# Performance work log

Hardware: AMD Instinct MI355X
Metric: run time of the kernel (lower is better)

## Reference

```python
import jax, jax.numpy as jnp
import numpy as np

EPS = 1e-8

def prelu(x, a):
    return jnp.where(x >= 0, x, a * x)

def setup_inputs() -> dict:
    key = jax.random.key(0)
    ks = jax.random.split(key, 8)
    B, G, N, T = 4, 8, 128, 6000
    H = 384
    x = jax.random.normal(ks[0], (B, G, N, T), dtype=jnp.float32)
    # torch.nn.Linear default init: U(-1/sqrt(fan_in), 1/sqrt(fan_in))
    def lin(k, out_f, in_f):
        k1, k2 = jax.random.split(k)
        bound = 1.0 / np.sqrt(in_f)
        W = jax.random.uniform(k1, (out_f, in_f), minval=-bound, maxval=bound, dtype=jnp.float32)
        b = jax.random.uniform(k2, (out_f,), minval=-bound, maxval=bound, dtype=jnp.float32)
        return W, b
    Wi, bi = lin(ks[1], H, N)
    Wm, bm = lin(ks[2], H, H)
    Wo, bo = lin(ks[3], N, 2 * H)
    # PReLU default: single learnable scalar initialized to 0.25
    ai = jnp.float32(0.25)
    am = jnp.float32(0.25)
    ao = jnp.float32(0.25)
    gamma = jnp.ones((N,), dtype=jnp.float32)
    beta = jnp.zeros((N,), dtype=jnp.float32)
    return {"input": x, "Wi": Wi, "bi": bi, "ai": ai, "Wm": Wm, "bm": bm, "am": am,
            "Wo": Wo, "bo": bo, "ao": ao, "gamma": gamma, "beta": beta}

def reference(input, Wi, bi, ai, Wm, bm, am, Wo, bo, ao, gamma, beta):
    B, G, N, T = input.shape
    # [B, T, G, N]
    h = jnp.transpose(input, (0, 3, 1, 2))
    # TAC_input: Linear(N->H) + PReLU
    gi = prelu(jnp.einsum('btgn,hn->btgh', h, Wi) + bi, ai)          # [B,T,G,H]
    # mean over groups, TAC_mean: Linear(H->H) + PReLU
    gm = gi.mean(axis=2)                                              # [B,T,H]
    gm = prelu(jnp.einsum('bth,oh->bto', gm, Wm) + bm, am)            # [B,T,H]
    gm = jnp.broadcast_to(gm[:, :, None, :], gi.shape)                # [B,T,G,H]
    cat = jnp.concatenate([gi, gm], axis=-1)                          # [B,T,G,2H]
    # TAC_output: Linear(2H->N) + PReLU
    go = prelu(jnp.einsum('btgc,nc->btgn', cat, Wo) + bo, ao)         # [B,T,G,N]
    go = jnp.transpose(go, (0, 2, 3, 1))                              # [B,G,N,T]
    # GlobLN over (N, T) per (batch*G) sample, affine along channel N
    mean = go.mean(axis=(2, 3), keepdims=True)
    var = jnp.mean((go - mean) ** 2, axis=(2, 3), keepdims=True)
    normed = (go - mean) / jnp.sqrt(var + EPS)
    go = gamma[None, None, :, None] * normed + beta[None, None, :, None]
    return input + go
```

## Files before the change

kernel.cpp:

```cpp
#include <hip/hip_runtime.h>

typedef __bf16 bf16_t;
typedef __bf16 bf16x8 __attribute__((ext_vector_type(8)));
typedef float f32x4 __attribute__((ext_vector_type(4)));

static constexpr int Bq = 4, Gg = 8, Nn = 128, Tt = 6000, Hh = 384;
static constexpr int TB = 16;
static constexpr int MR = TB * Gg;
static constexpr int LDA = 136;
static constexpr int LDG = 392;
static constexpr int LDSM = 392;
static constexpr int LDV = 132;

static constexpr size_t OFF_WI  = 0;
static constexpr size_t OFF_WM  = OFF_WI + (size_t)Hh * Nn * 2;
static constexpr size_t OFF_WO  = OFF_WM + (size_t)Hh * Hh * 2;
static constexpr size_t OFF_ST  = OFF_WO + (size_t)Nn * 2 * Hh * 2;
static constexpr size_t OFF_MRS = OFF_ST + 64 * 2 * 4;
static constexpr size_t OFF_GO  = (size_t)1 << 20;
static constexpr size_t WS_NEED = OFF_GO + (size_t)Bq * Tt * Gg * Nn * 2;

static constexpr int SM_SM = 0;
static constexpr int SM_MM = 12544;
static constexpr int SM_VV = 25088;
static constexpr int SM_GI = 34816;
static constexpr int SM_STT = 135168;
static constexpr int SMEM_BYTES = 135232;

#define MFMA16(a, b, c) __builtin_amdgcn_mfma_f32_16x16x32_bf16((a), (b), (c), 0, 0, 0)

__global__ void k0_prep(const float* __restrict__ Wi, const float* __restrict__ Wm,
                        const float* __restrict__ Wo,
                        bf16_t* __restrict__ WiB, bf16_t* __restrict__ WmB,
                        bf16_t* __restrict__ WoB, float* __restrict__ stats) {
    int i = blockIdx.x * blockDim.x + threadIdx.x;
    const int n1 = Hh * Nn, n2 = Hh * Hh, n3 = Nn * 2 * Hh;
    for (int idx = i; idx < n1 + n2 + n3; idx += gridDim.x * blockDim.x) {
        if (idx < n1)            WiB[idx] = (bf16_t)Wi[idx];
        else if (idx < n1 + n2)  WmB[idx - n1] = (bf16_t)Wm[idx - n1];
        else                     WoB[idx - n1 - n2] = (bf16_t)Wo[idx - n1 - n2];
    }
    if (i < 128) stats[i] = 0.f;
}

__device__ __forceinline__ int as_col(int row, int c) {
    return ((((c >> 3) ^ ((row >> 3) & 7)) << 3) | (c & 7));
}

__global__ __launch_bounds__(512, 2)
void k1_fused(const float* __restrict__ x,
              const bf16_t* __restrict__ WiB, const float* __restrict__ bi, const float* __restrict__ aip,
              const bf16_t* __restrict__ WmB, const float* __restrict__ bm, const float* __restrict__ amp,
              const bf16_t* __restrict__ WoB, const float* __restrict__ bo, const float* __restrict__ aop,
              bf16_t* __restrict__ go, float* __restrict__ stats) {
    extern __shared__ char smem[];
    bf16_t* As = (bf16_t*)(smem);
    bf16_t* Sm = (bf16_t*)(smem + SM_SM);
    bf16_t* Mm = (bf16_t*)(smem + SM_MM);
    float*  Vv = (float*)(smem + SM_VV);
    bf16_t* Gi = (bf16_t*)(smem + SM_GI);
    float*  st = (float*)(smem + SM_STT);

    const int tid  = threadIdx.x;
    const int lane = tid & 63;
    const int w    = tid >> 6;
    const int l15  = lane & 15;
    const int l4   = lane >> 4;
    const int mh   = w >> 2;
    const int ws4  = w & 3;
    const int b    = blockIdx.x / (Tt / TB);
    const int t0   = (blockIdx.x % (Tt / TB)) * TB;

    if (tid < 16) st[tid] = 0.f;

    for (int idx = tid; idx < MR * Nn; idx += 512) {
        int tl = idx & 15;
        int gn = idx >> 4;
        int g = gn >> 7;
        int n = gn & 127;
        float v = x[((size_t)((b * Gg + g) * Nn + n)) * Tt + t0 + tl];
        int row = tl * Gg + g;
        As[row * LDA + as_col(row, n)] = (bf16_t)v;
    }
    __syncthreads();

    const float ai = aip[0], am = amp[0], ao = aop[0];

    {
        const int cb = ws4 * 96;
        f32x4 acc[4][6];
        #pragma unroll
        for (int mt = 0; mt < 4; mt++)
            #pragma unroll
            for (int ni = 0; ni < 6; ni++) acc[mt][ni] = f32x4{0.f, 0.f, 0.f, 0.f};
        #pragma unroll
        for (int kk = 0; kk < 4; kk++) {
            const int k0 = kk * 32 + l4 * 8;
            bf16x8 a[4], bb[6];
            #pragma unroll
            for (int ni = 0; ni < 6; ni++)
                bb[ni] = *(const bf16x8*)&WiB[(cb + ni * 16 + l15) * Nn + k0];
            #pragma unroll
            for (int mt = 0; mt < 4; mt++) {
                int row = mh * 64 + mt * 16 + l15;
                a[mt] = *(const bf16x8*)&As[row * LDA + as_col(row, k0)];
            }
            #pragma unroll
            for (int mt = 0; mt < 4; mt++)
                #pragma unroll
                for (int ni = 0; ni < 6; ni++)
                    acc[mt][ni] = MFMA16(a[mt], bb[ni], acc[mt][ni]);
        }
        #pragma unroll
        for (int ni = 0; ni < 6; ni++) {
            int col = cb + ni * 16 + l15;
            float bv = bi[col];
            #pragma unroll
            for (int mt = 0; mt < 4; mt++) {
                #pragma unroll
                for (int j = 0; j < 4; j++) {
                    int row = mh * 64 + mt * 16 + l4 * 4 + j;
                    float v = acc[mt][ni][j] + bv;
                    v = v >= 0.f ? v : ai * v;
                    Gi[row * LDG + col] = (bf16_t)v;
                }
            }
        }
    }
    __syncthreads();

    for (int idx = tid; idx < TB * (Hh / 8); idx += 512) {
        int tl = idx / (Hh / 8);
        int h0 = (idx - tl * (Hh / 8)) * 8;
        float s[8];
        #pragma unroll
        for (int e = 0; e < 8; e++) s[e] = 0.f;
        #pragma unroll
        for (int g = 0; g < 8; g++) {
            bf16x8 vv = *(const bf16x8*)&Gi[(tl * 8 + g) * LDG + h0];
            #pragma unroll
            for (int e = 0; e < 8; e++) s[e] += (float)vv[e];
        }
        bf16x8 o;
        #pragma unroll
        for (int e = 0; e < 8; e++) o[e] = (bf16_t)(0.125f * s[e]);
        *(bf16x8*)&Sm[tl * LDSM + h0] = o;
    }
    __syncthreads();

    {
        const int cb2 = w * 48;
        f32x4 acc2[3];
        #pragma unroll
        for (int ni = 0; ni < 3; ni++) acc2[ni] = f32x4{0.f, 0.f, 0.f, 0.f};
        #pragma unroll
        for (int kk = 0; kk < 12; kk++) {
            const int k0 = kk * 32 + l4 * 8;
            bf16x8 a = *(const bf16x8*)&Sm[l15 * LDSM + k0];
            #pragma unroll
            for (int ni = 0; ni < 3; ni++) {
                bf16x8 bb = *(const bf16x8*)&WmB[(cb2 + ni * 16 + l15) * Hh + k0];
                acc2[ni] = MFMA16(a, bb, acc2[ni]);
            }
        }
        #pragma unroll
        for (int ni = 0; ni < 3; ni++) {
            int col = cb2 + ni * 16 + l15;
            float bv = bm[col];
            #pragma unroll
            for (int j = 0; j < 4; j++) {
                float v = acc2[ni][j] + bv;
                v = v >= 0.f ? v : am * v;
                Mm[(l4 * 4 + j) * LDSM + col] = (bf16_t)v;
            }
        }
    }
    __syncthreads();

    {
        const int nblk = w * 16;
        f32x4 acc3 = f32x4{0.f, 0.f, 0.f, 0.f};
        #pragma unroll
        for (int kk = 0; kk < 12; kk++) {
            const int k0 = kk * 32 + l4 * 8;
            bf16x8 a = *(const bf16x8*)&Mm[l15 * LDSM + k0];
            bf16x8 bb = *(const bf16x8*)&WoB[(nblk + l15) * 768 + 384 + k0];
            acc3 = MFMA16(a, bb, acc3);
        }
        #pragma unroll
        for (int j = 0; j < 4; j++) Vv[(l4 * 4 + j) * LDV + nblk + l15] = acc3[j];
    }
    __syncthreads();

    {
        const int cb4 = ws4 * 32;
        f32x4 acc4[4][2];
        #pragma unroll
        for (int mt = 0; mt < 4; mt++)
            #pragma unroll
            for (int ni = 0; ni < 2; ni++) acc4[mt][ni] = f32x4{0.f, 0.f, 0.f, 0.f};
        #pragma unroll
        for (int kk = 0; kk < 12; kk++) {
            const int k0 = kk * 32 + l4 * 8;
            bf16x8 b0 = *(const bf16x8*)&WoB[(cb4 + l15) * 768 + k0];
            bf16x8 b1 = *(const bf16x8*)&WoB[(cb4 + 16 + l15) * 768 + k0];
            bf16x8 a[4];
            #pragma unroll
            for (int mt = 0; mt < 4; mt++)
                a[mt] = *(const bf16x8*)&Gi[(mh * 64 + mt * 16 + l15) * LDG + k0];
            #pragma unroll
            for (int mt = 0; mt < 4; mt++) {
                acc4[mt][0] = MFMA16(a[mt], b0, acc4[mt][0]);
                acc4[mt][1] = MFMA16(a[mt], b1, acc4[mt][1]);
            }
        }
        float gsum[4] = {0.f, 0.f, 0.f, 0.f};
        float gss[4]  = {0.f, 0.f, 0.f, 0.f};
        #pragma unroll
        for (int ni = 0; ni < 2; ni++) {
            int col = cb4 + ni * 16 + l15;
            float bv = bo[col];
            #pragma unroll
            for (int mt = 0; mt < 4; mt++) {
                #pragma unroll
                for (int j = 0; j < 4; j++) {
                    int row = mh * 64 + mt * 16 + l4 * 4 + j;
                    int tl = row >> 3;
                    int g = row & 7;
                    float v = acc4[mt][ni][j] + Vv[tl * LDV + col] + bv;
                    v = v >= 0.f ? v : ao * v;
                    go[((size_t)((b * Tt + t0 + tl) * Gg + g)) * Nn + col] = (bf16_t)v;
                    gsum[j] += v;
                    gss[j] += v * v;
                }
            }
        }
        #pragma unroll
        for (int j = 0; j < 4; j++) {
            float s = gsum[j], q = gss[j];
            #pragma unroll
            for (int off = 1; off < 16; off <<= 1) {
                s += __shfl_xor(s, off, 64);
                q += __shfl_xor(q, off, 64);
            }
            if (l15 == 0) {
                int g = (l4 * 4 + j) & 7;
                atomicAdd(&st[g * 2 + 0], s);
                atomicAdd(&st[g * 2 + 1], q);
            }
        }
    }
    __syncthreads();
    if (tid < 16) atomicAdd(&stats[b * 16 + tid], st[tid]);
}

__global__ void k_final(const float* __restrict__ stats, float* __restrict__ mr) {
    int i = threadIdx.x;
    if (i < 64) {
        const float cnt = (float)Nn * (float)Tt;
        float mean = stats[i * 2] / cnt;
        float var = stats[i * 2 + 1] / cnt - mean * mean;
        mr[i * 2] = mean;
        mr[i * 2 + 1] = rsqrtf(var + 1e-8f);
    }
}

__global__ __launch_bounds__(256)
void k_apply(const float* __restrict__ x, const bf16_t* __restrict__ go,
             const float* __restrict__ mr, const float* __restrict__ gamma,
             const float* __restrict__ beta, float* __restrict__ out) {
    __shared__ float tr[32][65];
    int bid = blockIdx.x;
    const int tt = bid % 94; bid /= 94;
    const int nn = bid & 3;  bid >>= 2;
    const int g = bid & 7;
    const int b = bid >> 3;
    const int t0 = tt * 64, n0 = nn * 32;
    const int tid = threadIdx.x;
    const float mean = mr[(b * 8 + g) * 2], rstd = mr[(b * 8 + g) * 2 + 1];

    for (int idx = tid; idx < 2048; idx += 256) {
        int nl = idx & 31, tl = idx >> 5;
        int t = t0 + tl;
        float v = 0.f;
        if (t < Tt) v = (float)go[((size_t)((b * Tt + t) * Gg + g)) * Nn + n0 + nl];
        tr[nl][tl] = v;
    }
    __syncthreads();
    for (int idx = tid; idx < 2048; idx += 256) {
        int tl = idx & 63, nl = idx >> 6;
        int t = t0 + tl;
        if (t < Tt) {
            int n = n0 + nl;
            size_t a = ((size_t)((b * Gg + g) * Nn + n)) * Tt + t;
            out[a] = x[a] + gamma[n] * (tr[nl][tl] - mean) * rstd + beta[n];
        }
    }
}

extern "C" void kernel_launch(void* const* d_in, const int* in_sizes, int n_in,
                              void* d_out, int out_size, void* d_ws, size_t ws_size,
                              hipStream_t stream) {
    const float* x     = (const float*)d_in[0];
    const float* Wi    = (const float*)d_in[1];
    const float* bi    = (const float*)d_in[2];
    const float* ai    = (const float*)d_in[3];
    const float* Wm    = (const float*)d_in[4];
    const float* bm    = (const float*)d_in[5];
    const float* am    = (const float*)d_in[6];
    const float* Wo    = (const float*)d_in[7];
    const float* bo    = (const float*)d_in[8];
    const float* ao    = (const float*)d_in[9];
    const float* gamma = (const float*)d_in[10];
    const float* beta  = (const float*)d_in[11];
    float* out = (float*)d_out;
    char* ws = (char*)d_ws;

    if (ws_size < WS_NEED) return;

    bf16_t* WiB  = (bf16_t*)(ws + OFF_WI);
    bf16_t* WmB  = (bf16_t*)(ws + OFF_WM);
    bf16_t* WoB  = (bf16_t*)(ws + OFF_WO);
    float*  stat = (float*)(ws + OFF_ST);
    float*  mrs  = (float*)(ws + OFF_MRS);
    bf16_t* goB  = (bf16_t*)(ws + OFF_GO);

    k0_prep<<<dim3(512), dim3(256), 0, stream>>>(Wi, Wm, Wo, WiB, WmB, WoB, stat);
    k1_fused<<<dim3(Bq * (Tt / TB)), dim3(512), SMEM_BYTES, stream>>>(
        x, WiB, bi, ai, WmB, bm, am, WoB, bo, ao, goB, stat);
    k_final<<<dim3(1), dim3(64), 0, stream>>>(stat, mrs);
    k_apply<<<dim3(Bq * Gg * 4 * 94), dim3(256), 0, stream>>>(x, goB, mrs, gamma, beta, out);
}
```

Measured before the change: 254.8 us.

## Halve time tile per block and replace global atomics with per-block partial sums

Reduces the per-block time tile from 16 to 8 steps, which halves shared memory use and raises the occupancy target to 4 blocks per CU. It also doubles the block count, improving load balance. Small MFMA tiles in the mean and output stages now waste half their rows, and the weight matrices are re-read by twice as many blocks. Global atomic accumulation of the norm statistics is replaced by per-block partial writes, reduced in a single 1024-thread final kernel, which also removes the stats zeroing from the prep kernel.

```diff
diff --git a/kernel.cpp b/kernel.cpp
--- a/kernel.cpp
+++ b/kernel.cpp
@@ -5,8 +5,9 @@
 typedef float f32x4 __attribute__((ext_vector_type(4)));
 
 static constexpr int Bq = 4, Gg = 8, Nn = 128, Tt = 6000, Hh = 384;
-static constexpr int TB = 16;
+static constexpr int TB = 8;
 static constexpr int MR = TB * Gg;
+static constexpr int NBLK = Tt / TB;
 static constexpr int LDA = 136;
 static constexpr int LDG = 392;
 static constexpr int LDSM = 392;
@@ -15,24 +16,24 @@
 static constexpr size_t OFF_WI  = 0;
 static constexpr size_t OFF_WM  = OFF_WI + (size_t)Hh * Nn * 2;
 static constexpr size_t OFF_WO  = OFF_WM + (size_t)Hh * Hh * 2;
-static constexpr size_t OFF_ST  = OFF_WO + (size_t)Nn * 2 * Hh * 2;
-static constexpr size_t OFF_MRS = OFF_ST + 64 * 2 * 4;
+static constexpr size_t OFF_PT  = OFF_WO + (size_t)Nn * 2 * Hh * 2;
+static constexpr size_t OFF_MRS = OFF_PT + (size_t)Bq * NBLK * 16 * 4;
 static constexpr size_t OFF_GO  = (size_t)1 << 20;
 static constexpr size_t WS_NEED = OFF_GO + (size_t)Bq * Tt * Gg * Nn * 2;
 
-static constexpr int SM_SM = 0;
-static constexpr int SM_MM = 12544;
-static constexpr int SM_VV = 25088;
-static constexpr int SM_GI = 34816;
-static constexpr int SM_STT = 135168;
-static constexpr int SMEM_BYTES = 135232;
+static constexpr int SM_SM  = 0;
+static constexpr int SM_MM  = 6272;
+static constexpr int SM_VV  = 12544;
+static constexpr int SM_GI  = 17408;
+static constexpr int SM_STT = 67584;
+static constexpr int SMEM_BYTES = 67648;
 
 #define MFMA16(a, b, c) __builtin_amdgcn_mfma_f32_16x16x32_bf16((a), (b), (c), 0, 0, 0)
 
 __global__ void k0_prep(const float* __restrict__ Wi, const float* __restrict__ Wm,
                         const float* __restrict__ Wo,
                         bf16_t* __restrict__ WiB, bf16_t* __restrict__ WmB,
-                        bf16_t* __restrict__ WoB, float* __restrict__ stats) {
+                        bf16_t* __restrict__ WoB) {
     int i = blockIdx.x * blockDim.x + threadIdx.x;
     const int n1 = Hh * Nn, n2 = Hh * Hh, n3 = Nn * 2 * Hh;
     for (int idx = i; idx < n1 + n2 + n3; idx += gridDim.x * blockDim.x) {
@@ -40,19 +41,18 @@
         else if (idx < n1 + n2)  WmB[idx - n1] = (bf16_t)Wm[idx - n1];
         else                     WoB[idx - n1 - n2] = (bf16_t)Wo[idx - n1 - n2];
     }
-    if (i < 128) stats[i] = 0.f;
 }
 
 __device__ __forceinline__ int as_col(int row, int c) {
     return ((((c >> 3) ^ ((row >> 3) & 7)) << 3) | (c & 7));
 }
 
-__global__ __launch_bounds__(512, 2)
+__global__ __launch_bounds__(512, 4)
 void k1_fused(const float* __restrict__ x,
               const bf16_t* __restrict__ WiB, const float* __restrict__ bi, const float* __restrict__ aip,
               const bf16_t* __restrict__ WmB, const float* __restrict__ bm, const float* __restrict__ amp,
               const bf16_t* __restrict__ WoB, const float* __restrict__ bo, const float* __restrict__ aop,
-              bf16_t* __restrict__ go, float* __restrict__ stats) {
+              bf16_t* __restrict__ go, float* __restrict__ part) {
     extern __shared__ char smem[];
     bf16_t* As = (bf16_t*)(smem);
     bf16_t* Sm = (bf16_t*)(smem + SM_SM);
@@ -68,14 +68,14 @@
     const int l4   = lane >> 4;
     const int mh   = w >> 2;
     const int ws4  = w & 3;
-    const int b    = blockIdx.x / (Tt / TB);
-    const int t0   = (blockIdx.x % (Tt / TB)) * TB;
+    const int b    = blockIdx.x / NBLK;
+    const int t0   = (blockIdx.x % NBLK) * TB;
 
     if (tid < 16) st[tid] = 0.f;
 
     for (int idx = tid; idx < MR * Nn; idx += 512) {
-        int tl = idx & 15;
-        int gn = idx >> 4;
+        int tl = idx & 7;
+        int gn = idx >> 3;
         int g = gn >> 7;
         int n = gn & 127;
         float v = x[((size_t)((b * Gg + g) * Nn + n)) * Tt + t0 + tl];
@@ -88,25 +88,25 @@
 
     {
         const int cb = ws4 * 96;
-        f32x4 acc[4][6];
-        #pragma unroll
-        for (int mt = 0; mt < 4; mt++)
+        f32x4 acc[2][6];
+        #pragma unroll
+        for (int mt = 0; mt < 2; mt++)
             #pragma unroll
             for (int ni = 0; ni < 6; ni++) acc[mt][ni] = f32x4{0.f, 0.f, 0.f, 0.f};
         #pragma unroll
         for (int kk = 0; kk < 4; kk++) {
             const int k0 = kk * 32 + l4 * 8;
-            bf16x8 a[4], bb[6];
+            bf16x8 a[2], bb[6];
             #pragma unroll
             for (int ni = 0; ni < 6; ni++)
                 bb[ni] = *(const bf16x8*)&WiB[(cb + ni * 16 + l15) * Nn + k0];
             #pragma unroll
-            for (int mt = 0; mt < 4; mt++) {
-                int row = mh * 64 + mt * 16 + l15;
+            for (int mt = 0; mt < 2; mt++) {
+                int row = mh * 32 + mt * 16 + l15;
                 a[mt] = *(const bf16x8*)&As[row * LDA + as_col(row, k0)];
             }
             #pragma unroll
-            for (int mt = 0; mt < 4; mt++)
+            for (int mt = 0; mt < 2; mt++)
                 #pragma unroll
                 for (int ni = 0; ni < 6; ni++)
                     acc[mt][ni] = MFMA16(a[mt], bb[ni], acc[mt][ni]);
@@ -116,10 +116,10 @@
             int col = cb + ni * 16 + l15;
             float bv = bi[col];
             #pragma unroll
-            for (int mt = 0; mt < 4; mt++) {
+            for (int mt = 0; mt < 2; mt++) {
                 #pragma unroll
                 for (int j = 0; j < 4; j++) {
-                    int row = mh * 64 + mt * 16 + l4 * 4 + j;
+                    int row = mh * 32 + mt * 16 + l4 * 4 + j;
                     float v = acc[mt][ni][j] + bv;
                     v = v >= 0.f ? v : ai * v;
                     Gi[row * LDG + col] = (bf16_t)v;
@@ -156,22 +156,24 @@
         #pragma unroll
         for (int kk = 0; kk < 12; kk++) {
             const int k0 = kk * 32 + l4 * 8;
-            bf16x8 a = *(const bf16x8*)&Sm[l15 * LDSM + k0];
+            bf16x8 a = *(const bf16x8*)&Sm[(l15 & 7) * LDSM + k0];
             #pragma unroll
             for (int ni = 0; ni < 3; ni++) {
                 bf16x8 bb = *(const bf16x8*)&WmB[(cb2 + ni * 16 + l15) * Hh + k0];
                 acc2[ni] = MFMA16(a, bb, acc2[ni]);
             }
         }
-        #pragma unroll
-        for (int ni = 0; ni < 3; ni++) {
-            int col = cb2 + ni * 16 + l15;
-            float bv = bm[col];
-            #pragma unroll
-            for (int j = 0; j < 4; j++) {
-                float v = acc2[ni][j] + bv;
-                v = v >= 0.f ? v : am * v;
-                Mm[(l4 * 4 + j) * LDSM + col] = (bf16_t)v;
+        if (l4 < 2) {
+            #pragma unroll
+            for (int ni = 0; ni < 3; ni++) {
+                int col = cb2 + ni * 16 + l15;
+                float bv = bm[col];
+                #pragma unroll
+                for (int j = 0; j < 4; j++) {
+                    float v = acc2[ni][j] + bv;
+                    v = v >= 0.f ? v : am * v;
+                    Mm[(l4 * 4 + j) * LDSM + col] = (bf16_t)v;
+                }
             }
         }
     }
@@ -183,20 +185,22 @@
         #pragma unroll
         for (int kk = 0; kk < 12; kk++) {
             const int k0 = kk * 32 + l4 * 8;
-            bf16x8 a = *(const bf16x8*)&Mm[l15 * LDSM + k0];
+            bf16x8 a = *(const bf16x8*)&Mm[(l15 & 7) * LDSM + k0];
             bf16x8 bb = *(const bf16x8*)&WoB[(nblk + l15) * 768 + 384 + k0];
             acc3 = MFMA16(a, bb, acc3);
         }
-        #pragma unroll
-        for (int j = 0; j < 4; j++) Vv[(l4 * 4 + j) * LDV + nblk + l15] = acc3[j];
+        if (l4 < 2) {
+            #pragma unroll
+            for (int j = 0; j < 4; j++) Vv[(l4 * 4 + j) * LDV + nblk + l15] = acc3[j];
+        }
     }
     __syncthreads();
 
     {
         const int cb4 = ws4 * 32;
-        f32x4 acc4[4][2];
-        #pragma unroll
-        for (int mt = 0; mt < 4; mt++)
+        f32x4 acc4[2][2];
+        #pragma unroll
+        for (int mt = 0; mt < 2; mt++)
             #pragma unroll
             for (int ni = 0; ni < 2; ni++) acc4[mt][ni] = f32x4{0.f, 0.f, 0.f, 0.f};
         #pragma unroll
@@ -204,12 +208,12 @@
             const int k0 = kk * 32 + l4 * 8;
             bf16x8 b0 = *(const bf16x8*)&WoB[(cb4 + l15) * 768 + k0];
             bf16x8 b1 = *(const bf16x8*)&WoB[(cb4 + 16 + l15) * 768 + k0];
-            bf16x8 a[4];
-            #pragma unroll
-            for (int mt = 0; mt < 4; mt++)
-                a[mt] = *(const bf16x8*)&Gi[(mh * 64 + mt * 16 + l15) * LDG + k0];
-            #pragma unroll
-            for (int mt = 0; mt < 4; mt++) {
+            bf16x8 a[2];
+            #pragma unroll
+            for (int mt = 0; mt < 2; mt++)
+                a[mt] = *(const bf16x8*)&Gi[(mh * 32 + mt * 16 + l15) * LDG + k0];
+            #pragma unroll
+            for (int mt = 0; mt < 2; mt++) {
                 acc4[mt][0] = MFMA16(a[mt], b0, acc4[mt][0]);
                 acc4[mt][1] = MFMA16(a[mt], b1, acc4[mt][1]);
             }
@@ -221,10 +225,10 @@
             int col = cb4 + ni * 16 + l15;
             float bv = bo[col];
             #pragma unroll
-            for (int mt = 0; mt < 4; mt++) {
+            for (int mt = 0; mt < 2; mt++) {
                 #pragma unroll
                 for (int j = 0; j < 4; j++) {
-                    int row = mh * 64 + mt * 16 + l4 * 4 + j;
+                    int row = mh * 32 + mt * 16 + l4 * 4 + j;
                     int tl = row >> 3;
                     int g = row & 7;
                     float v = acc4[mt][ni][j] + Vv[tl * LDV + col] + bv;
@@ -251,17 +255,39 @@
         }
     }
     __syncthreads();
-    if (tid < 16) atomicAdd(&stats[b * 16 + tid], st[tid]);
-}
-
-__global__ void k_final(const float* __restrict__ stats, float* __restrict__ mr) {
-    int i = threadIdx.x;
-    if (i < 64) {
-        const float cnt = (float)Nn * (float)Tt;
-        float mean = stats[i * 2] / cnt;
-        float var = stats[i * 2 + 1] / cnt - mean * mean;
-        mr[i * 2] = mean;
-        mr[i * 2 + 1] = rsqrtf(var + 1e-8f);
+    if (tid < 16) part[(size_t)blockIdx.x * 16 + tid] = st[tid];
+}
+
+__global__ __launch_bounds__(1024)
+void k_final(const float* __restrict__ part, float* __restrict__ mr) {
+    __shared__ float red[64][17];
+    const int tid = threadIdx.x;
+    const int key = tid & 63;
+    const int chunk = tid >> 6;
+    const int bb = key >> 4;
+    const int t0 = chunk * 47;
+    const int cnt = min(47, NBLK - t0);
+    float s = 0.f;
+    for (int i = 0; i < cnt; i++)
+        s += part[(size_t)(bb * NBLK + t0 + i) * 16 + (key & 15)];
+    red[key][chunk] = s;
+    __syncthreads();
+    if (tid < 64) {
+        float tot = 0.f;
+        #pragma unroll
+        for (int ch = 0; ch < 16; ch++) tot += red[tid][ch];
+        red[tid][16] = tot;
+    }
+    __syncthreads();
+    if (tid < 32) {
+        int b2 = tid >> 3, g2 = tid & 7;
+        float s0 = red[b2 * 16 + g2 * 2][16];
+        float s1 = red[b2 * 16 + g2 * 2 + 1][16];
+        const float cntf = (float)Nn * (float)Tt;
+        float mean = s0 / cntf;
+        float var = s1 / cntf - mean * mean;
+        mr[tid * 2] = mean;
+        mr[tid * 2 + 1] = rsqrtf(var + 1e-8f);
     }
 }
 
@@ -321,13 +347,13 @@
     bf16_t* WiB  = (bf16_t*)(ws + OFF_WI);
     bf16_t* WmB  = (bf16_t*)(ws + OFF_WM);
     bf16_t* WoB  = (bf16_t*)(ws + OFF_WO);
-    float*  stat = (float*)(ws + OFF_ST);
+    float*  prt  = (float*)(ws + OFF_PT);
     float*  mrs  = (float*)(ws + OFF_MRS);
     bf16_t* goB  = (bf16_t*)(ws + OFF_GO);
 
-    k0_prep<<<dim3(512), dim3(256), 0, stream>>>(Wi, Wm, Wo, WiB, WmB, WoB, stat);
-    k1_fused<<<dim3(Bq * (Tt / TB)), dim3(512), SMEM_BYTES, stream>>>(
-        x, WiB, bi, ai, WmB, bm, am, WoB, bo, ao, goB, stat);
-    k_final<<<dim3(1), dim3(64), 0, stream>>>(stat, mrs);
+    k0_prep<<<dim3(512), dim3(256), 0, stream>>>(Wi, Wm, Wo, WiB, WmB, WoB);
+    k1_fused<<<dim3(Bq * NBLK), dim3(512), SMEM_BYTES, stream>>>(
+        x, WiB, bi, ai, WmB, bm, am, WoB, bo, ao, goB, prt);
+    k_final<<<dim3(1), dim3(1024), 0, stream>>>(prt, mrs);
     k_apply<<<dim3(Bq * Gg * 4 * 94), dim3(256), 0, stream>>>(x, goB, mrs, gamma, beta, out);
 }
```

Measured after the change: 367.4 us. +44.1%, slower.

## Split fused TAC kernel into three GEMM stages with global intermediates

Applied to the files above, without the earlier changes.

Replaces the single large-shared-memory fused kernel with three kernels: first-layer GEMM plus group mean, a mid kernel for the mean-branch GEMMs, and the output GEMM that writes per-tile partial statistics instead of atomics. Intermediates gi, gm and v now go through global workspace, processed in chunks sized to the available workspace, with the old fused path kept as a fallback. The aim is to free LDS and raise occupancy and MFMA utilisation per stage, at the cost of extra global traffic for the gi intermediate and more launches.

```diff
diff --git a/kernel.cpp b/kernel.cpp
--- a/kernel.cpp
+++ b/kernel.cpp
@@ -6,26 +6,23 @@
 
 static constexpr int Bq = 4, Gg = 8, Nn = 128, Tt = 6000, Hh = 384;
 static constexpr int TB = 16;
-static constexpr int MR = TB * Gg;
+static constexpr int NTPB = Tt / TB;
+static constexpr int NTILES = Bq * NTPB;
 static constexpr int LDA = 136;
-static constexpr int LDG = 392;
-static constexpr int LDSM = 392;
-static constexpr int LDV = 132;
+static constexpr int LDMM = 392;
 
 static constexpr size_t OFF_WI  = 0;
 static constexpr size_t OFF_WM  = OFF_WI + (size_t)Hh * Nn * 2;
 static constexpr size_t OFF_WO  = OFF_WM + (size_t)Hh * Hh * 2;
-static constexpr size_t OFF_ST  = OFF_WO + (size_t)Nn * 2 * Hh * 2;
-static constexpr size_t OFF_MRS = OFF_ST + 64 * 2 * 4;
-static constexpr size_t OFF_GO  = (size_t)1 << 20;
-static constexpr size_t WS_NEED = OFF_GO + (size_t)Bq * Tt * Gg * Nn * 2;
-
-static constexpr int SM_SM = 0;
-static constexpr int SM_MM = 12544;
-static constexpr int SM_VV = 25088;
-static constexpr int SM_GI = 34816;
-static constexpr int SM_STT = 135168;
-static constexpr int SMEM_BYTES = 135232;
+static constexpr size_t OFF_PT  = OFF_WO + (size_t)Nn * 2 * Hh * 2;
+static constexpr size_t OFF_MRS = OFF_PT + (size_t)NTILES * 4 * 16 * 4;
+static constexpr size_t OFF_GM  = (size_t)1 << 20;
+static constexpr size_t OFF_V   = OFF_GM + (size_t)Bq * Tt * Hh * 2;
+static constexpr size_t OFF_GO  = OFF_V + (size_t)Bq * Tt * Nn * 4;
+static constexpr size_t OFF_GI  = OFF_GO + (size_t)Bq * Tt * Gg * Nn * 2;
+static constexpr size_t GI_BYTES_FULL = (size_t)NTILES * 128 * Hh * 2;
+static constexpr size_t OFF_GO_FB = (size_t)1 << 20;
+static constexpr size_t WS_FB = OFF_GO_FB + (size_t)Bq * Tt * Gg * Nn * 2;
 
 #define MFMA16(a, b, c) __builtin_amdgcn_mfma_f32_16x16x32_bf16((a), (b), (c), 0, 0, 0)
 
@@ -47,221 +44,237 @@
     return ((((c >> 3) ^ ((row >> 3) & 7)) << 3) | (c & 7));
 }
 
-__global__ __launch_bounds__(512, 2)
-void k1_fused(const float* __restrict__ x,
-              const bf16_t* __restrict__ WiB, const float* __restrict__ bi, const float* __restrict__ aip,
-              const bf16_t* __restrict__ WmB, const float* __restrict__ bm, const float* __restrict__ amp,
-              const bf16_t* __restrict__ WoB, const float* __restrict__ bo, const float* __restrict__ aop,
-              bf16_t* __restrict__ go, float* __restrict__ stats) {
-    extern __shared__ char smem[];
-    bf16_t* As = (bf16_t*)(smem);
-    bf16_t* Sm = (bf16_t*)(smem + SM_SM);
-    bf16_t* Mm = (bf16_t*)(smem + SM_MM);
-    float*  Vv = (float*)(smem + SM_VV);
-    bf16_t* Gi = (bf16_t*)(smem + SM_GI);
-    float*  st = (float*)(smem + SM_STT);
-
-    const int tid  = threadIdx.x;
-    const int lane = tid & 63;
-    const int w    = tid >> 6;
-    const int l15  = lane & 15;
-    const int l4   = lane >> 4;
-    const int mh   = w >> 2;
-    const int ws4  = w & 3;
-    const int b    = blockIdx.x / (Tt / TB);
-    const int t0   = (blockIdx.x % (Tt / TB)) * TB;
-
-    if (tid < 16) st[tid] = 0.f;
-
-    for (int idx = tid; idx < MR * Nn; idx += 512) {
-        int tl = idx & 15;
-        int gn = idx >> 4;
-        int g = gn >> 7;
-        int n = gn & 127;
-        float v = x[((size_t)((b * Gg + g) * Nn + n)) * Tt + t0 + tl];
-        int row = tl * Gg + g;
-        As[row * LDA + as_col(row, n)] = (bf16_t)v;
-    }
-    __syncthreads();
-
-    const float ai = aip[0], am = amp[0], ao = aop[0];
+__global__ __launch_bounds__(512, 4)
+void kA_gemm1(const float* __restrict__ x, const bf16_t* __restrict__ WiB,
+              const float* __restrict__ bi, const float* __restrict__ aip,
+              bf16_t* __restrict__ gi, bf16_t* __restrict__ gm, int tile0) {
+    __shared__ bf16_t As[128 * LDA];
+    const int tid = threadIdx.x, lane = tid & 63, w = tid >> 6;
+    const int l15 = lane & 15, l4 = lane >> 4;
+    const int tile = tile0 + blockIdx.x;
+    const int b = tile / NTPB, t0 = (tile % NTPB) * TB;
 
     {
-        const int cb = ws4 * 96;
-        f32x4 acc[4][6];
-        #pragma unroll
-        for (int mt = 0; mt < 4; mt++)
-            #pragma unroll
-            for (int ni = 0; ni < 6; ni++) acc[mt][ni] = f32x4{0.f, 0.f, 0.f, 0.f};
-        #pragma unroll
-        for (int kk = 0; kk < 4; kk++) {
-            const int k0 = kk * 32 + l4 * 8;
-            bf16x8 a[4], bb[6];
-            #pragma unroll
-            for (int ni = 0; ni < 6; ni++)
-                bb[ni] = *(const bf16x8*)&WiB[(cb + ni * 16 + l15) * Nn + k0];
-            #pragma unroll
-            for (int mt = 0; mt < 4; mt++) {
-                int row = mh * 64 + mt * 16 + l15;
-                a[mt] = *(const bf16x8*)&As[row * LDA + as_col(row, k0)];
-            }
-            #pragma unroll
-            for (int mt = 0; mt < 4; mt++)
+        const int g0 = tid >> 7, n0 = tid & 127;
+        #pragma unroll
+        for (int h = 0; h < 2; h++) {
+            int gg = g0 + 4 * h;
+            #pragma unroll
+            for (int q = 0; q < 4; q++) {
+                f32x4 xv = *(const f32x4*)&x[((size_t)((b * Gg + gg) * Nn + n0)) * Tt + t0 + 4 * q];
                 #pragma unroll
-                for (int ni = 0; ni < 6; ni++)
-                    acc[mt][ni] = MFMA16(a[mt], bb[ni], acc[mt][ni]);
-        }
-        #pragma unroll
-        for (int ni = 0; ni < 6; ni++) {
-            int col = cb + ni * 16 + l15;
-            float bv = bi[col];
-            #pragma unroll
-            for (int mt = 0; mt < 4; mt++) {
-                #pragma unroll
-                for (int j = 0; j < 4; j++) {
-                    int row = mh * 64 + mt * 16 + l4 * 4 + j;
-                    float v = acc[mt][ni][j] + bv;
-                    v = v >= 0.f ? v : ai * v;
-                    Gi[row * LDG + col] = (bf16_t)v;
+                for (int e = 0; e < 4; e++) {
+                    int row = (q * 4 + e) * Gg + gg;
+                    As[row * LDA + as_col(row, n0)] = (bf16_t)xv[e];
                 }
             }
         }
     }
     __syncthreads();
 
-    for (int idx = tid; idx < TB * (Hh / 8); idx += 512) {
-        int tl = idx / (Hh / 8);
-        int h0 = (idx - tl * (Hh / 8)) * 8;
-        float s[8];
-        #pragma unroll
-        for (int e = 0; e < 8; e++) s[e] = 0.f;
-        #pragma unroll
-        for (int g = 0; g < 8; g++) {
-            bf16x8 vv = *(const bf16x8*)&Gi[(tl * 8 + g) * LDG + h0];
-            #pragma unroll
-            for (int e = 0; e < 8; e++) s[e] += (float)vv[e];
-        }
-        bf16x8 o;
-        #pragma unroll
-        for (int e = 0; e < 8; e++) o[e] = (bf16_t)(0.125f * s[e]);
-        *(bf16x8*)&Sm[tl * LDSM + h0] = o;
-    }
-    __syncthreads();
-
-    {
-        const int cb2 = w * 48;
-        f32x4 acc2[3];
-        #pragma unroll
-        for (int ni = 0; ni < 3; ni++) acc2[ni] = f32x4{0.f, 0.f, 0.f, 0.f};
-        #pragma unroll
-        for (int kk = 0; kk < 12; kk++) {
-            const int k0 = kk * 32 + l4 * 8;
-            bf16x8 a = *(const bf16x8*)&Sm[l15 * LDSM + k0];
-            #pragma unroll
-            for (int ni = 0; ni < 3; ni++) {
-                bf16x8 bb = *(const bf16x8*)&WmB[(cb2 + ni * 16 + l15) * Hh + k0];
-                acc2[ni] = MFMA16(a, bb, acc2[ni]);
-            }
-        }
-        #pragma unroll
-        for (int ni = 0; ni < 3; ni++) {
-            int col = cb2 + ni * 16 + l15;
-            float bv = bm[col];
+    const float ai = aip[0];
+    const int cb = w * 48;
+    f32x4 acc[8][3];
+    #pragma unroll
+    for (int mt = 0; mt < 8; mt++)
+        #pragma unroll
+        for (int nc = 0; nc < 3; nc++) acc[mt][nc] = f32x4{0.f, 0.f, 0.f, 0.f};
+    #pragma unroll
+    for (int kk = 0; kk < 4; kk++) {
+        const int k0 = kk * 32 + l4 * 8;
+        bf16x8 bb[3];
+        #pragma unroll
+        for (int nc = 0; nc < 3; nc++)
+            bb[nc] = *(const bf16x8*)&WiB[(cb + nc * 16 + l15) * Nn + k0];
+        #pragma unroll
+        for (int mt = 0; mt < 8; mt++) {
+            int row = mt * 16 + l15;
+            bf16x8 a = *(const bf16x8*)&As[row * LDA + as_col(row, k0)];
+            #pragma unroll
+            for (int nc = 0; nc < 3; nc++) acc[mt][nc] = MFMA16(a, bb[nc], acc[mt][nc]);
+        }
+    }
+    const size_t giBase = (size_t)blockIdx.x * 128 * Hh;
+    #pragma unroll
+    for (int nc = 0; nc < 3; nc++) {
+        int col = cb + nc * 16 + l15;
+        float bv = bi[col];
+        #pragma unroll
+        for (int mt = 0; mt < 8; mt++) {
+            float ms = 0.f;
             #pragma unroll
             for (int j = 0; j < 4; j++) {
-                float v = acc2[ni][j] + bv;
-                v = v >= 0.f ? v : am * v;
-                Mm[(l4 * 4 + j) * LDSM + col] = (bf16_t)v;
-            }
-        }
-    }
-    __syncthreads();
-
-    {
-        const int nblk = w * 16;
-        f32x4 acc3 = f32x4{0.f, 0.f, 0.f, 0.f};
-        #pragma unroll
-        for (int kk = 0; kk < 12; kk++) {
-            const int k0 = kk * 32 + l4 * 8;
-            bf16x8 a = *(const bf16x8*)&Mm[l15 * LDSM + k0];
-            bf16x8 bb = *(const bf16x8*)&WoB[(nblk + l15) * 768 + 384 + k0];
-            acc3 = MFMA16(a, bb, acc3);
-        }
-        #pragma unroll
-        for (int j = 0; j < 4; j++) Vv[(l4 * 4 + j) * LDV + nblk + l15] = acc3[j];
-    }
-    __syncthreads();
-
-    {
-        const int cb4 = ws4 * 32;
-        f32x4 acc4[4][2];
-        #pragma unroll
-        for (int mt = 0; mt < 4; mt++)
-            #pragma unroll
-            for (int ni = 0; ni < 2; ni++) acc4[mt][ni] = f32x4{0.f, 0.f, 0.f, 0.f};
-        #pragma unroll
-        for (int kk = 0; kk < 12; kk++) {
-            const int k0 = kk * 32 + l4 * 8;
-            bf16x8 b0 = *(const bf16x8*)&WoB[(cb4 + l15) * 768 + k0];
-            bf16x8 b1 = *(const bf16x8*)&WoB[(cb4 + 16 + l15) * 768 + k0];
-            bf16x8 a[4];
-            #pragma unroll
-            for (int mt = 0; mt < 4; mt++)
-                a[mt] = *(const bf16x8*)&Gi[(mh * 64 + mt * 16 + l15) * LDG + k0];
-            #pragma unroll
-            for (int mt = 0; mt < 4; mt++) {
-                acc4[mt][0] = MFMA16(a[mt], b0, acc4[mt][0]);
-                acc4[mt][1] = MFMA16(a[mt], b1, acc4[mt][1]);
-            }
-        }
-        float gsum[4] = {0.f, 0.f, 0.f, 0.f};
-        float gss[4]  = {0.f, 0.f, 0.f, 0.f};
-        #pragma unroll
-        for (int ni = 0; ni < 2; ni++) {
-            int col = cb4 + ni * 16 + l15;
-            float bv = bo[col];
-            #pragma unroll
-            for (int mt = 0; mt < 4; mt++) {
-                #pragma unroll
-                for (int j = 0; j < 4; j++) {
-                    int row = mh * 64 + mt * 16 + l4 * 4 + j;
-                    int tl = row >> 3;
-                    int g = row & 7;
-                    float v = acc4[mt][ni][j] + Vv[tl * LDV + col] + bv;
-                    v = v >= 0.f ? v : ao * v;
-                    go[((size_t)((b * Tt + t0 + tl) * Gg + g)) * Nn + col] = (bf16_t)v;
-                    gsum[j] += v;
-                    gss[j] += v * v;
-                }
-            }
-        }
+                int row = mt * 16 + l4 * 4 + j;
+                float v = acc[mt][nc][j] + bv;
+                v = v >= 0.f ? v : ai * v;
+                gi[giBase + (size_t)row * Hh + col] = (bf16_t)v;
+                ms += v;
+            }
+            ms += __shfl_xor(ms, 16, 64);
+            if ((l4 & 1) == 0) {
+                int tl = mt * 2 + (l4 >> 1);
+                gm[((size_t)tile * TB + tl) * Hh + col] = (bf16_t)(0.125f * ms);
+            }
+        }
+    }
+}
+
+__global__ __launch_bounds__(256, 2)
+void kB_mid(const bf16_t* __restrict__ gm, const bf16_t* __restrict__ WmB,
+            const float* __restrict__ bm, const float* __restrict__ amp,
+            const bf16_t* __restrict__ WoB, float* __restrict__ v,
+            int tile0, int ntilesC) {
+    __shared__ bf16_t MmS[4][16 * LDMM];
+    const int tid = threadIdx.x, lane = tid & 63, w = tid >> 6;
+    const int l15 = lane & 15, l4 = lane >> 4;
+    const int tileL = blockIdx.x * 4 + w;
+    if (tileL >= ntilesC) return;
+    const int row0 = (tile0 + tileL) * TB;
+    bf16_t* Mm = MmS[w];
+
+    f32x4 acc2[24];
+    #pragma unroll
+    for (int nc = 0; nc < 24; nc++) acc2[nc] = f32x4{0.f, 0.f, 0.f, 0.f};
+    #pragma unroll
+    for (int ks = 0; ks < 12; ks++) {
+        const int k0 = ks * 32 + l4 * 8;
+        bf16x8 a = *(const bf16x8*)&gm[((size_t)row0 + l15) * Hh + k0];
+        #pragma unroll
+        for (int nc = 0; nc < 24; nc++) {
+            bf16x8 bb = *(const bf16x8*)&WmB[(nc * 16 + l15) * Hh + k0];
+            acc2[nc] = MFMA16(a, bb, acc2[nc]);
+        }
+    }
+    const float am = amp[0];
+    #pragma unroll
+    for (int nc = 0; nc < 24; nc++) {
+        int col = nc * 16 + l15;
+        float bv = bm[col];
         #pragma unroll
         for (int j = 0; j < 4; j++) {
-            float s = gsum[j], q = gss[j];
-            #pragma unroll
-            for (int off = 1; off < 16; off <<= 1) {
-                s += __shfl_xor(s, off, 64);
-                q += __shfl_xor(q, off, 64);
-            }
-            if (l15 == 0) {
-                int g = (l4 * 4 + j) & 7;
-                atomicAdd(&st[g * 2 + 0], s);
-                atomicAdd(&st[g * 2 + 1], q);
-            }
-        }
-    }
-    __syncthreads();
-    if (tid < 16) atomicAdd(&stats[b * 16 + tid], st[tid]);
-}
-
-__global__ void k_final(const float* __restrict__ stats, float* __restrict__ mr) {
-    int i = threadIdx.x;
-    if (i < 64) {
-        const float cnt = (float)Nn * (float)Tt;
-        float mean = stats[i * 2] / cnt;
-        float var = stats[i * 2 + 1] / cnt - mean * mean;
-        mr[i * 2] = mean;
-        mr[i * 2 + 1] = rsqrtf(var + 1e-8f);
+            float vv = acc2[nc][j] + bv;
+            vv = vv >= 0.f ? vv : am * vv;
+            Mm[(l4 * 4 + j) * LDMM + col] = (bf16_t)vv;
+        }
+    }
+    f32x4 acc3[8];
+    #pragma unroll
+    for (int nc = 0; nc < 8; nc++) acc3[nc] = f32x4{0.f, 0.f, 0.f, 0.f};
+    #pragma unroll
+    for (int ks = 0; ks < 12; ks++) {
+        const int k0 = ks * 32 + l4 * 8;
+        bf16x8 a = *(const bf16x8*)&Mm[l15 * LDMM + k0];
+        #pragma unroll
+        for (int nc = 0; nc < 8; nc++) {
+            bf16x8 bb = *(const bf16x8*)&WoB[(nc * 16 + l15) * 768 + 384 + k0];
+            acc3[nc] = MFMA16(a, bb, acc3[nc]);
+        }
+    }
+    #pragma unroll
+    for (int nc = 0; nc < 8; nc++) {
+        int col = nc * 16 + l15;
+        #pragma unroll
+        for (int j = 0; j < 4; j++)
+            v[((size_t)row0 + l4 * 4 + j) * Nn + col] = acc3[nc][j];
+    }
+}
+
+__global__ __launch_bounds__(256, 3)
+void kC_gemm4(const bf16_t* __restrict__ gi, const float* __restrict__ v,
+              const bf16_t* __restrict__ WoB, const float* __restrict__ bo,
+              const float* __restrict__ aop, bf16_t* __restrict__ go,
+              float* __restrict__ part, int tile0) {
+    const int tid = threadIdx.x, lane = tid & 63, w = tid >> 6;
+    const int l15 = lane & 15, l4 = lane >> 4;
+    const int tile = tile0 + blockIdx.x;
+    const size_t rL0 = (size_t)blockIdx.x * 128 + w * 32;
+    const size_t Rg0 = (size_t)tile * 128 + w * 32;
+
+    f32x4 acc[2][8];
+    #pragma unroll
+    for (int mt = 0; mt < 2; mt++)
+        #pragma unroll
+        for (int nc = 0; nc < 8; nc++) acc[mt][nc] = f32x4{0.f, 0.f, 0.f, 0.f};
+    #pragma unroll
+    for (int ks = 0; ks < 12; ks++) {
+        const int k0 = ks * 32 + l4 * 8;
+        bf16x8 bb[8];
+        #pragma unroll
+        for (int nc = 0; nc < 8; nc++)
+            bb[nc] = *(const bf16x8*)&WoB[(nc * 16 + l15) * 768 + k0];
+        #pragma unroll
+        for (int mt = 0; mt < 2; mt++) {
+            bf16x8 a = *(const bf16x8*)&gi[(rL0 + mt * 16 + l15) * Hh + k0];
+            #pragma unroll
+            for (int nc = 0; nc < 8; nc++) acc[mt][nc] = MFMA16(a, bb[nc], acc[mt][nc]);
+        }
+    }
+    const float ao = aop[0];
+    float gsum[4] = {0.f, 0.f, 0.f, 0.f};
+    float gss[4]  = {0.f, 0.f, 0.f, 0.f};
+    #pragma unroll
+    for (int nc = 0; nc < 8; nc++) {
+        int col = nc * 16 + l15;
+        float bv = bo[col];
+        #pragma unroll
+        for (int mt = 0; mt < 2; mt++) {
+            #pragma unroll
+            for (int j = 0; j < 4; j++) {
+                size_t Rg = Rg0 + mt * 16 + l4 * 4 + j;
+                float val = acc[mt][nc][j] + v[(Rg >> 3) * Nn + col] + bv;
+                val = val >= 0.f ? val : ao * val;
+                go[Rg * Nn + col] = (bf16_t)val;
+                gsum[j] += val;
+                gss[j] += val * val;
+            }
+        }
+    }
+    #pragma unroll
+    for (int j = 0; j < 4; j++) {
+        float s = gsum[j], q = gss[j];
+        #pragma unroll
+        for (int off = 1; off < 16; off <<= 1) {
+            s += __shfl_xor(s, off, 64);
+            q += __shfl_xor(q, off, 64);
+        }
+        s += __shfl_xor(s, 32, 64);
+        q += __shfl_xor(q, 32, 64);
+        if (l15 == 0 && l4 < 2) {
+            int g = l4 * 4 + j;
+            part[((size_t)tile * 4 + w) * 16 + g * 2 + 0] = s;
+            part[((size_t)tile * 4 + w) * 16 + g * 2 + 1] = q;
+        }
+    }
+}
+
+__global__ __launch_bounds__(1024)
+void k_final_split(const float* __restrict__ part, float* __restrict__ mr) {
+    __shared__ float red[64][17];
+    const int tid = threadIdx.x, key = tid & 63, chunk = tid >> 6;
+    const int bb = key >> 4;
+    const int t0 = chunk * 94;
+    const int cnt = min(94, 1500 - t0);
+    float s = 0.f;
+    for (int i = 0; i < cnt; i++)
+        s += part[(size_t)(bb * 1500 + t0 + i) * 16 + (key & 15)];
+    red[key][chunk] = s;
+    __syncthreads();
+    if (tid < 64) {
+        float tot = 0.f;
+        #pragma unroll
+        for (int ch = 0; ch < 16; ch++) tot += red[tid][ch];
+        red[tid][16] = tot;
+    }
+    __syncthreads();
+    if (tid < 32) {
+        int b2 = tid >> 3, g2 = tid & 7;
+        float s0 = red[b2 * 16 + g2 * 2][16];
+        float s1 = red[b2 * 16 + g2 * 2 + 1][16];
+        const float cntf = (float)Nn * (float)Tt;
+        float mean = s0 / cntf;
+        float var = s1 / cntf - mean * mean;
+        mr[tid * 2] = mean;
+        mr[tid * 2 + 1] = rsqrtf(var + 1e-8f);
     }
 }
 
@@ -295,6 +308,206 @@
             size_t a = ((size_t)((b * Gg + g) * Nn + n)) * Tt + t;
             out[a] = x[a] + gamma[n] * (tr[nl][tl] - mean) * rstd + beta[n];
         }
+    }
+}
+
+static constexpr int FB_LDA = 136, FB_LDG = 392, FB_LDSM = 392, FB_LDV = 132;
+static constexpr int FB_SM_SM = 0, FB_SM_MM = 12544, FB_SM_VV = 25088,
+                     FB_SM_GI = 34816, FB_SM_STT = 135168, FB_SMEM = 135232;
+
+__global__ __launch_bounds__(512, 2)
+void k1_fused_fb(const float* __restrict__ x,
+                 const bf16_t* __restrict__ WiB, const float* __restrict__ bi, const float* __restrict__ aip,
+                 const bf16_t* __restrict__ WmB, const float* __restrict__ bm, const float* __restrict__ amp,
+                 const bf16_t* __restrict__ WoB, const float* __restrict__ bo, const float* __restrict__ aop,
+                 bf16_t* __restrict__ go, float* __restrict__ stats) {
+    extern __shared__ char smem[];
+    bf16_t* As = (bf16_t*)(smem);
+    bf16_t* Sm = (bf16_t*)(smem + FB_SM_SM);
+    bf16_t* Mm = (bf16_t*)(smem + FB_SM_MM);
+    float*  Vv = (float*)(smem + FB_SM_VV);
+    bf16_t* Gi = (bf16_t*)(smem + FB_SM_GI);
+    float*  st = (float*)(smem + FB_SM_STT);
+    const int tid = threadIdx.x, lane = tid & 63, w = tid >> 6;
+    const int l15 = lane & 15, l4 = lane >> 4, mh = w >> 2, ws4 = w & 3;
+    const int b = blockIdx.x / NTPB, t0 = (blockIdx.x % NTPB) * TB;
+    if (tid < 16) st[tid] = 0.f;
+    for (int idx = tid; idx < 128 * Nn; idx += 512) {
+        int tl = idx & 15, gn = idx >> 4, g = gn >> 7, n = gn & 127;
+        float v = x[((size_t)((b * Gg + g) * Nn + n)) * Tt + t0 + tl];
+        int row = tl * Gg + g;
+        As[row * FB_LDA + as_col(row, n)] = (bf16_t)v;
+    }
+    __syncthreads();
+    const float ai = aip[0], am = amp[0], ao = aop[0];
+    {
+        const int cb = ws4 * 96;
+        f32x4 acc[4][6];
+        #pragma unroll
+        for (int mt = 0; mt < 4; mt++)
+            #pragma unroll
+            for (int ni = 0; ni < 6; ni++) acc[mt][ni] = f32x4{0.f, 0.f, 0.f, 0.f};
+        #pragma unroll
+        for (int kk = 0; kk < 4; kk++) {
+            const int k0 = kk * 32 + l4 * 8;
+            bf16x8 a[4], bb[6];
+            #pragma unroll
+            for (int ni = 0; ni < 6; ni++)
+                bb[ni] = *(const bf16x8*)&WiB[(cb + ni * 16 + l15) * Nn + k0];
+            #pragma unroll
+            for (int mt = 0; mt < 4; mt++) {
+                int row = mh * 64 + mt * 16 + l15;
+                a[mt] = *(const bf16x8*)&As[row * FB_LDA + as_col(row, k0)];
+            }
+            #pragma unroll
+            for (int mt = 0; mt < 4; mt++)
+                #pragma unroll
+                for (int ni = 0; ni < 6; ni++)
+                    acc[mt][ni] = MFMA16(a[mt], bb[ni], acc[mt][ni]);
+        }
+        #pragma unroll
+        for (int ni = 0; ni < 6; ni++) {
+            int col = cb + ni * 16 + l15;
+            float bv = bi[col];
+            #pragma unroll
+            for (int mt = 0; mt < 4; mt++)
+                #pragma unroll
+                for (int j = 0; j < 4; j++) {
+                    int row = mh * 64 + mt * 16 + l4 * 4 + j;
+                    float v = acc[mt][ni][j] + bv;
+                    v = v >= 0.f ? v : ai * v;
+                    Gi[row * FB_LDG + col] = (bf16_t)v;
+                }
+        }
+    }
+    __syncthreads();
+    for (int idx = tid; idx < TB * (Hh / 8); idx += 512) {
+        int tl = idx / (Hh / 8), h0 = (idx - tl * (Hh / 8)) * 8;
+        float s[8];
+        #pragma unroll
+        for (int e = 0; e < 8; e++) s[e] = 0.f;
+        #pragma unroll
+        for (int g = 0; g < 8; g++) {
+            bf16x8 vv = *(const bf16x8*)&Gi[(tl * 8 + g) * FB_LDG + h0];
+            #pragma unroll
+            for (int e = 0; e < 8; e++) s[e] += (float)vv[e];
+        }
+        bf16x8 o;
+        #pragma unroll
+        for (int e = 0; e < 8; e++) o[e] = (bf16_t)(0.125f * s[e]);
+        *(bf16x8*)&Sm[tl * FB_LDSM + h0] = o;
+    }
+    __syncthreads();
+    {
+        const int cb2 = w * 48;
+        f32x4 acc2[3];
+        #pragma unroll
+        for (int ni = 0; ni < 3; ni++) acc2[ni] = f32x4{0.f, 0.f, 0.f, 0.f};
+        #pragma unroll
+        for (int kk = 0; kk < 12; kk++) {
+            const int k0 = kk * 32 + l4 * 8;
+            bf16x8 a = *(const bf16x8*)&Sm[l15 * FB_LDSM + k0];
+            #pragma unroll
+            for (int ni = 0; ni < 3; ni++) {
+                bf16x8 bb = *(const bf16x8*)&WmB[(cb2 + ni * 16 + l15) * Hh + k0];
+                acc2[ni] = MFMA16(a, bb, acc2[ni]);
+            }
+        }
+        #pragma unroll
+        for (int ni = 0; ni < 3; ni++) {
+            int col = cb2 + ni * 16 + l15;
+            float bv = bm[col];
+            #pragma unroll
+            for (int j = 0; j < 4; j++) {
+                float v = acc2[ni][j] + bv;
+                v = v >= 0.f ? v : am * v;
+                Mm[(l4 * 4 + j) * FB_LDSM + col] = (bf16_t)v;
+            }
+        }
+    }
+    __syncthreads();
+    {
+        const int nblk = w * 16;
+        f32x4 acc3 = f32x4{0.f, 0.f, 0.f, 0.f};
+        #pragma unroll
+        for (int kk = 0; kk < 12; kk++) {
+            const int k0 = kk * 32 + l4 * 8;
+            bf16x8 a = *(const bf16x8*)&Mm[l15 * FB_LDSM + k0];
+            bf16x8 bb = *(const bf16x8*)&WoB[(nblk + l15) * 768 + 384 + k0];
+            acc3 = MFMA16(a, bb, acc3);
+        }
+        #pragma unroll
+        for (int j = 0; j < 4; j++) Vv[(l4 * 4 + j) * FB_LDV + nblk + l15] = acc3[j];
+    }
+    __syncthreads();
+    {
+        const int cb4 = ws4 * 32;
+        f32x4 acc4[4][2];
+        #pragma unroll
+        for (int mt = 0; mt < 4; mt++)
+            #pragma unroll
+            for (int ni = 0; ni < 2; ni++) acc4[mt][ni] = f32x4{0.f, 0.f, 0.f, 0.f};
+        #pragma unroll
+        for (int kk = 0; kk < 12; kk++) {
+            const int k0 = kk * 32 + l4 * 8;
+            bf16x8 b0 = *(const bf16x8*)&WoB[(cb4 + l15) * 768 + k0];
+            bf16x8 b1 = *(const bf16x8*)&WoB[(cb4 + 16 + l15) * 768 + k0];
+            bf16x8 a[4];
+            #pragma unroll
+            for (int mt = 0; mt < 4; mt++)
+                a[mt] = *(const bf16x8*)&Gi[(mh * 64 + mt * 16 + l15) * FB_LDG + k0];
+            #pragma unroll
+            for (int mt = 0; mt < 4; mt++) {
+                acc4[mt][0] = MFMA16(a[mt], b0, acc4[mt][0]);
+                acc4[mt][1] = MFMA16(a[mt], b1, acc4[mt][1]);
+            }
+        }
+        float gsum[4] = {0.f, 0.f, 0.f, 0.f};
+        float gss[4]  = {0.f, 0.f, 0.f, 0.f};
+        #pragma unroll
+        for (int ni = 0; ni < 2; ni++) {
+            int col = cb4 + ni * 16 + l15;
+            float bv = bo[col];
+            #pragma unroll
+            for (int mt = 0; mt < 4; mt++)
+                #pragma unroll
+                for (int j = 0; j < 4; j++) {
+                    int row = mh * 64 + mt * 16 + l4 * 4 + j;
+                    int tl = row >> 3, g = row & 7;
+                    float v = acc4[mt][ni][j] + Vv[tl * FB_LDV + col] + bv;
+                    v = v >= 0.f ? v : ao * v;
+                    go[((size_t)((b * Tt + t0 + tl) * Gg + g)) * Nn + col] = (bf16_t)v;
+                    gsum[j] += v;
+                    gss[j] += v * v;
+                }
+        }
+        #pragma unroll
+        for (int j = 0; j < 4; j++) {
+            float s = gsum[j], q = gss[j];
+            #pragma unroll
+            for (int off = 1; off < 16; off <<= 1) {
+                s += __shfl_xor(s, off, 64);
+                q += __shfl_xor(q, off, 64);
+            }
+            if (l15 == 0) {
+                int g = (l4 * 4 + j) & 7;
+                atomicAdd(&st[g * 2 + 0], s);
+                atomicAdd(&st[g * 2 + 1], q);
+            }
+        }
+    }
+    __syncthreads();
+    if (tid < 16) atomicAdd(&stats[b * 16 + tid], st[tid]);
+}
+
+__global__ void k_final_fb(const float* __restrict__ stats, float* __restrict__ mr) {
+    int i = threadIdx.x;
+    if (i < 32) {
+        const float cnt = (float)Nn * (float)Tt;
+        float mean = stats[i * 2] / cnt;
+        float var = stats[i * 2 + 1] / cnt - mean * mean;
+        mr[i * 2] = mean;
+        mr[i * 2 + 1] = rsqrtf(var + 1e-8f);
     }
 }
 
@@ -316,18 +529,39 @@
     float* out = (float*)d_out;
     char* ws = (char*)d_ws;
 
-    if (ws_size < WS_NEED) return;
-
-    bf16_t* WiB  = (bf16_t*)(ws + OFF_WI);
-    bf16_t* WmB  = (bf16_t*)(ws + OFF_WM);
-    bf16_t* WoB  = (bf16_t*)(ws + OFF_WO);
-    float*  stat = (float*)(ws + OFF_ST);
-    float*  mrs  = (float*)(ws + OFF_MRS);
-    bf16_t* goB  = (bf16_t*)(ws + OFF_GO);
-
-    k0_prep<<<dim3(512), dim3(256), 0, stream>>>(Wi, Wm, Wo, WiB, WmB, WoB, stat);
-    k1_fused<<<dim3(Bq * (Tt / TB)), dim3(512), SMEM_BYTES, stream>>>(
-        x, WiB, bi, ai, WmB, bm, am, WoB, bo, ao, goB, stat);
-    k_final<<<dim3(1), dim3(64), 0, stream>>>(stat, mrs);
-    k_apply<<<dim3(Bq * Gg * 4 * 94), dim3(256), 0, stream>>>(x, goB, mrs, gamma, beta, out);
-}
+    bf16_t* WiB = (bf16_t*)(ws + OFF_WI);
+    bf16_t* WmB = (bf16_t*)(ws + OFF_WM);
+    bf16_t* WoB = (bf16_t*)(ws + OFF_WO);
+    float*  prt = (float*)(ws + OFF_PT);
+    float*  mrs = (float*)(ws + OFF_MRS);
+
+    int nch = 0;
+    if      (ws_size >= OFF_GI + GI_BYTES_FULL)     nch = 1;
+    else if (ws_size >= OFF_GI + GI_BYTES_FULL / 2) nch = 2;
+    else if (ws_size >= OFF_GI + GI_BYTES_FULL / 4) nch = 4;
+
+    if (nch) {
+        bf16_t* gm  = (bf16_t*)(ws + OFF_GM);
+        float*  vv  = (float*)(ws + OFF_V);
+        bf16_t* goB = (bf16_t*)(ws + OFF_GO);
+        bf16_t* gic = (bf16_t*)(ws + OFF_GI);
+        const int tpc = NTILES / nch;
+
+        k0_prep<<<dim3(512), dim3(256), 0, stream>>>(Wi, Wm, Wo, WiB, WmB, WoB, prt);
+        for (int c = 0; c < nch; c++) {
+            const int tile0 = c * tpc;
+            kA_gemm1<<<dim3(tpc), dim3(512), 0, stream>>>(x, WiB, bi, ai, gic, gm, tile0);
+            kB_mid<<<dim3((tpc + 3) / 4), dim3(256), 0, stream>>>(gm, WmB, bm, am, WoB, vv, tile0, tpc);
+            kC_gemm4<<<dim3(tpc), dim3(256), 0, stream>>>(gic, vv, WoB, bo, ao, goB, prt, tile0);
+        }
+        k_final_split<<<dim3(1), dim3(1024), 0, stream>>>(prt, mrs);
+        k_apply<<<dim3(Bq * Gg * 4 * 94), dim3(256), 0, stream>>>(x, goB, mrs, gamma, beta, out);
+    } else if (ws_size >= WS_FB) {
+        bf16_t* goB = (bf16_t*)(ws + OFF_GO_FB);
+        k0_prep<<<dim3(512), dim3(256), 0, stream>>>(Wi, Wm, Wo, WiB, WmB, WoB, prt);
+        k1_fused_fb<<<dim3(NTILES), dim3(512), FB_SMEM, stream>>>(
+            x, WiB, bi, ai, WmB, bm, am, WoB, bo, ao, goB, prt);
+        k_final_fb<<<dim3(1), dim3(64), 0, stream>>>(prt, mrs);
+        k_apply<<<dim3(Bq * Gg * 4 * 94), dim3(256), 0, stream>>>(x, goB, mrs, gamma, beta, out);
+    }
+}
```

Result: slower. 506.2 us (+98.6%).
